# Kernel tuning notes

Hardware: AMD Instinct MI355X
Metric: run time of the kernel (lower is better)

The kernel has to match this reference:

```python
import jax, jax.numpy as jnp
import numpy as np

B, S, IN_DIM = 8, 2048, 8
EMB, HEADS, NCLS = 512, 8, 3
HDIM = EMB // HEADS
HALF = EMB // 2


def setup_inputs() -> dict:
    key = jax.random.key(0)
    ks = jax.random.split(key, 16)
    g = lambda k, shp, fan_in: jax.random.normal(k, shp, jnp.float32) / np.sqrt(fan_in)
    return {
        "features": jax.random.normal(ks[0], (B, S, IN_DIM), jnp.float32),
        "timestamps": jax.random.uniform(ks[1], (B, S, 1), jnp.float32),
        # FeatureEmbedding
        "Wf": g(ks[2], (IN_DIM, EMB), IN_DIM), "bf": jnp.zeros((EMB,), jnp.float32),
        # Time2Vec
        "Wl": g(ks[3], (1, HALF), 1), "bl": jnp.zeros((HALF,), jnp.float32),
        "Wp": g(ks[4], (1, HALF), 1), "bp": jnp.zeros((HALF,), jnp.float32),
        # TimeAwareAttention
        "Wq": g(ks[5], (EMB, EMB), EMB), "bq": jnp.zeros((EMB,), jnp.float32),
        "Wk": g(ks[6], (EMB, EMB), EMB), "bk": jnp.zeros((EMB,), jnp.float32),
        "Wv": g(ks[7], (EMB, EMB), EMB), "bv": jnp.zeros((EMB,), jnp.float32),
        "Wo": g(ks[8], (EMB, EMB), EMB), "bo": jnp.zeros((EMB,), jnp.float32),
        "time_decay": jnp.ones((1,), jnp.float32),
        # Classifier MLP (dropout is identity in eval)
        "W1": g(ks[9], (EMB, EMB // 2), EMB), "b1": jnp.zeros((EMB // 2,), jnp.float32),
        "W2": g(ks[10], (EMB // 2, NCLS), EMB // 2), "b2": jnp.zeros((NCLS,), jnp.float32),
    }


def reference(features, timestamps, Wf, bf, Wl, bl, Wp, bp,
              Wq, bq, Wk, bk, Wv, bv, Wo, bo, time_decay, W1, b1, W2, b2):
    # embeddings: feature linear + Time2Vec(linear || sin(linear))
    feat_emb = features @ Wf + bf                              # [B,S,E]
    time_emb = jnp.concatenate(
        [timestamps @ Wl + bl, jnp.sin(timestamps @ Wp + bp)], axis=-1)
    x = feat_emb + time_emb                                    # [B,S,E]

    # pairwise time-decay weights: exp(-decay * |t_i - t_j|)  [B,S,S]
    t = timestamps[..., 0]
    decay = jnp.exp(-time_decay[0] * jnp.abs(t[:, :, None] - t[:, None, :]))

    def split_heads(y):  # [B,S,E] -> [B,H,S,D]
        return y.reshape(B, S, HEADS, HDIM).transpose(0, 2, 1, 3)

    q = split_heads(x @ Wq + bq)
    k = split_heads(x @ Wk + bk)
    v = split_heads(x @ Wv + bv)

    scores = jnp.einsum('bhsd,bhtd->bhst', q, k) / np.sqrt(HDIM).astype(np.float32)
    scores = scores * decay[:, None, :, :]                     # elementwise decay bias
    attn = jax.nn.softmax(scores, axis=-1)
    out = jnp.einsum('bhst,bhtd->bhsd', attn, v)               # [B,H,S,D]
    out = out.transpose(0, 2, 1, 3).reshape(B, S, EMB)
    out = out @ Wo + bo

    h = out[:, -1, :]                                          # last token
    h = jax.nn.relu(h @ W1 + b1)
    logits = h @ W2 + b2                                       # [B,NCLS]
    return logits
```

## Files before the change

kernel.cpp:

```cpp
#include <hip/hip_runtime.h>
#include <hip/hip_bf16.h>
#include <math.h>

#define B 8
#define S 2048
#define IN_DIM 8
#define EMB 512
#define HEADS 8
#define HDIM 64
#define HALF 256
#define NCLS 3
#define NCHUNK 32

#define WS_KQ    0
#define WS_COEF1 32768
#define WS_PM    33536
#define WS_PS    66304
#define WS_OH    590592
#define WS_OP    594688

__global__ __launch_bounds__(256) void k_head(
    const float* __restrict__ feat, const float* __restrict__ ts,
    const float* __restrict__ Wf, const float* __restrict__ bf,
    const float* __restrict__ Wl, const float* __restrict__ bl,
    const float* __restrict__ Wp, const float* __restrict__ bp,
    const float* __restrict__ Wq, const float* __restrict__ bq,
    const float* __restrict__ Wk, const float* __restrict__ bk,
    float* __restrict__ ws)
{
    const int h = blockIdx.x;
    const int b = blockIdx.y;
    const int bh = b*HEADS + h;
    const int tid = threadIdx.x;
    __shared__ float xl[EMB];
    __shared__ __align__(16) float qc[HDIM];
    __shared__ float kq[EMB];
    __shared__ float red[4][64];
    __shared__ float red10[4][12];

    {
        const float tl = ts[b*S + (S-1)];
        float fv[IN_DIM];
        #pragma unroll
        for (int i = 0; i < IN_DIM; ++i) fv[i] = feat[(b*S + (S-1))*IN_DIM + i];
        #pragma unroll
        for (int r = 0; r < 2; ++r) {
            const int e = tid + r*256;
            float acc = bf[e];
            #pragma unroll
            for (int i = 0; i < IN_DIM; ++i) acc += fv[i]*Wf[i*EMB + e];
            if (r == 0) acc += tl*Wl[e] + bl[e];
            else        acc += __sinf(tl*Wp[e-HALF] + bp[e-HALF]);
            xl[e] = acc;
        }
    }
    __syncthreads();
    {
        const int eo = tid & 63, jq = tid >> 6;
        float acc = (jq == 0) ? bq[h*HDIM + eo] : 0.f;
        #pragma unroll 8
        for (int j = jq*128; j < jq*128 + 128; ++j)
            acc += xl[j]*Wq[j*EMB + h*HDIM + eo];
        red[jq][eo] = acc;
    }
    __syncthreads();
    if (tid < HDIM) qc[tid] = red[0][tid]+red[1][tid]+red[2][tid]+red[3][tid];
    __syncthreads();
    {
        #pragma unroll
        for (int r = 0; r < 2; ++r) {
            const int j = tid + r*256;
            const float4* wr = (const float4*)(Wk + j*EMB + h*HDIM);
            const float4* qv = (const float4*)qc;
            float acc = 0.f;
            #pragma unroll
            for (int k = 0; k < 16; ++k) {
                const float4 w = wr[k], q4 = qv[k];
                acc += w.x*q4.x + w.y*q4.y + w.z*q4.z + w.w*q4.w;
            }
            kq[j] = acc;
            if (j >= HALF) ws[WS_KQ + bh*EMB + j] = acc;
        }
    }
    __syncthreads();
    {
        float a[IN_DIM] = {0.f,0.f,0.f,0.f,0.f,0.f,0.f,0.f};
        float c0 = 0.f, c1 = 0.f;
        #pragma unroll
        for (int r = 0; r < 2; ++r) {
            const int e = tid + r*256;
            const float kv = kq[e];
            #pragma unroll
            for (int i = 0; i < IN_DIM; ++i) a[i] += Wf[i*EMB + e]*kv;
            c0 += bf[e]*kv;
            if (r == 0) { c0 += bl[e]*kv; c1 += Wl[e]*kv; }
        }
        if (tid < HDIM) c0 += qc[tid]*bk[h*HDIM + tid];
        #pragma unroll
        for (int off = 32; off >= 1; off >>= 1) {
            #pragma unroll
            for (int i = 0; i < IN_DIM; ++i) a[i] += __shfl_xor(a[i], off, 64);
            c0 += __shfl_xor(c0, off, 64);
            c1 += __shfl_xor(c1, off, 64);
        }
        const int wid = tid >> 6, lane = tid & 63;
        if (lane == 0) {
            #pragma unroll
            for (int i = 0; i < IN_DIM; ++i) red10[wid][i] = a[i];
            red10[wid][8] = c0; red10[wid][9] = c1;
        }
        __syncthreads();
        if (tid < 10)
            ws[WS_COEF1 + bh*12 + tid] =
                red10[0][tid]+red10[1][tid]+red10[2][tid]+red10[3][tid];
    }
}

__global__ __launch_bounds__(256) void k_part(
    const float* __restrict__ feat, const float* __restrict__ ts,
    const float* __restrict__ Wp, const float* __restrict__ bp,
    const float* __restrict__ tdp, float* __restrict__ ws)
{
    const int c = blockIdx.x;
    const int b = blockIdx.y;
    const int tid = threadIdx.x;
    const int t0 = c*64;

    __shared__ float sin_l[256*65];
    __shared__ __align__(16) float kqh[HEADS][256];
    __shared__ __align__(16) float w_l[64*8];
    __shared__ float tv_l[64];
    __shared__ float f_l[64*9];
    __shared__ float cf[96];

    if (tid < 64) tv_l[tid] = ts[b*S + t0 + tid];
    for (int idx = tid; idx < 64*IN_DIM; idx += 256) {
        const int tt = idx >> 3, i = idx & 7;
        f_l[tt*9 + i] = feat[(b*S + t0 + tt)*IN_DIM + i];
    }
    for (int idx = tid; idx < HEADS*256; idx += 256)
        ((float*)kqh)[idx] = ws[WS_KQ + (b*HEADS + (idx >> 8))*EMB + HALF + (idx & 255)];
    if (tid < 96) cf[tid] = ws[WS_COEF1 + b*96 + tid];
    const float tl = ts[b*S + (S-1)];
    const float td = tdp[0];
    __syncthreads();

    {
        const float wj = Wp[tid], bj = bp[tid];
        float* srow = sin_l + tid*65;
        #pragma unroll 4
        for (int tt = 0; tt < 64; ++tt)
            srow[tt] = __sinf(tv_l[tt]*wj + bj);
    }
    __syncthreads();

    const int t = tid & 63, h0 = tid >> 6;
    const float tv = tv_l[t];
    float fv[IN_DIM];
    #pragma unroll
    for (int i = 0; i < IN_DIM; ++i) fv[i] = f_l[t*9 + i];
    const float dec = __expf(-td*fabsf(tl - tv));
    float sc[2];
    {
        float acc0 = 0.f, acc1 = 0.f;
        const float4* kq0 = (const float4*)&kqh[h0][0];
        const float4* kq1 = (const float4*)&kqh[h0+4][0];
        #pragma unroll 4
        for (int j4 = 0; j4 < 64; ++j4) {
            const float s0 = sin_l[(j4*4+0)*65 + t];
            const float s1 = sin_l[(j4*4+1)*65 + t];
            const float s2 = sin_l[(j4*4+2)*65 + t];
            const float s3 = sin_l[(j4*4+3)*65 + t];
            const float4 ka = kq0[j4], kb = kq1[j4];
            acc0 += s0*ka.x + s1*ka.y + s2*ka.z + s3*ka.w;
            acc1 += s0*kb.x + s1*kb.y + s2*kb.z + s3*kb.w;
        }
        #pragma unroll
        for (int p = 0; p < 2; ++p) {
            const int h = h0 + p*4;
            float base = cf[h*12+8] + tv*cf[h*12+9];
            #pragma unroll
            for (int i = 0; i < IN_DIM; ++i) base += fv[i]*cf[h*12+i];
            sc[p] = (base + ((p == 0) ? acc0 : acc1))*0.125f*dec;
        }
    }
    #pragma unroll
    for (int p = 0; p < 2; ++p) {
        const int h = h0 + p*4;
        float m = sc[p];
        #pragma unroll
        for (int off = 32; off >= 1; off >>= 1) m = fmaxf(m, __shfl_xor(m, off, 64));
        const float w = __expf(sc[p] - m);
        float Z = w, ta = w*tv;
        float fa[IN_DIM];
        #pragma unroll
        for (int i = 0; i < IN_DIM; ++i) fa[i] = w*fv[i];
        #pragma unroll
        for (int off = 32; off >= 1; off >>= 1) {
            Z  += __shfl_xor(Z,  off, 64);
            ta += __shfl_xor(ta, off, 64);
            #pragma unroll
            for (int i = 0; i < IN_DIM; ++i) fa[i] += __shfl_xor(fa[i], off, 64);
        }
        w_l[t*8 + h] = w;
        if (t == 0) {
            float* pm = ws + WS_PM + ((b*NCHUNK + c)*HEADS + h)*16;
            pm[0] = m; pm[1] = Z; pm[2] = ta;
            #pragma unroll
            for (int i = 0; i < IN_DIM; ++i) pm[3+i] = fa[i];
        }
    }
    __syncthreads();
    {
        const int j = tid;
        float accS[HEADS] = {0.f,0.f,0.f,0.f,0.f,0.f,0.f,0.f};
        const float4* wv4 = (const float4*)w_l;
        const float* scol = sin_l + j*65;
        #pragma unroll 4
        for (int tt = 0; tt < 64; ++tt) {
            const float sv = scol[tt];
            const float4 wa = wv4[tt*2], wb = wv4[tt*2+1];
            accS[0] += wa.x*sv; accS[1] += wa.y*sv; accS[2] += wa.z*sv; accS[3] += wa.w*sv;
            accS[4] += wb.x*sv; accS[5] += wb.y*sv; accS[6] += wb.z*sv; accS[7] += wb.w*sv;
        }
        const int base = WS_PS + ((b*NCHUNK + c)*HEADS)*256 + j;
        #pragma unroll
        for (int h = 0; h < HEADS; ++h) ws[base + h*256] = accS[h];
    }
}

__global__ __launch_bounds__(256) void k_ohc(
    const float* __restrict__ Wf, const float* __restrict__ bf,
    const float* __restrict__ Wl, const float* __restrict__ bl,
    const float* __restrict__ Wv, const float* __restrict__ bv,
    const float* __restrict__ ws_, float* __restrict__ ws)
{
    const int h = blockIdx.x;
    const int b = blockIdx.y;
    const int tid = threadIdx.x;
    __shared__ float pm[NCHUNK][12];
    __shared__ float al[NCHUNK];
    __shared__ float cf[10];
    __shared__ float wx[EMB];
    __shared__ float red[4][64];

    for (int idx = tid; idx < NCHUNK*12; idx += 256) {
        const int c = idx / 12, k = idx % 12;
        pm[c][k] = (k < 11) ? ws_[WS_PM + ((b*NCHUNK + c)*HEADS + h)*16 + k] : 0.f;
    }
    __syncthreads();
    float m = pm[0][0];
    #pragma unroll 8
    for (int c = 1; c < NCHUNK; ++c) m = fmaxf(m, pm[c][0]);
    if (tid < NCHUNK) al[tid] = __expf(pm[tid][0] - m);
    __syncthreads();
    float Z = 0.f;
    #pragma unroll 8
    for (int c = 0; c < NCHUNK; ++c) Z += al[c]*pm[c][1];
    const float inv = 1.f/Z;
    if (tid < 9) {
        const int k = (tid == 8) ? 2 : 3 + tid;
        float acc = 0.f;
        #pragma unroll 8
        for (int c = 0; c < NCHUNK; ++c) acc += al[c]*pm[c][k];
        cf[(tid == 8) ? 8 : tid] = acc*inv;
    }
    __syncthreads();
    {
        const int j = tid;
        float acc = 0.f;
        #pragma unroll 8
        for (int c = 0; c < NCHUNK; ++c)
            acc += al[c]*ws_[WS_PS + ((b*NCHUNK + c)*HEADS + h)*256 + j];
        float vh = bf[HALF + j] + acc*inv;
        float vl = bf[j] + cf[8]*Wl[j] + bl[j];
        #pragma unroll
        for (int i = 0; i < IN_DIM; ++i) {
            vh += cf[i]*Wf[i*EMB + HALF + j];
            vl += cf[i]*Wf[i*EMB + j];
        }
        wx[j] = vl;
        wx[HALF + j] = vh;
    }
    __syncthreads();
    {
        const int eo = tid & 63, jq = tid >> 6;
        const int e = h*HDIM + eo;
        float acc = 0.f;
        #pragma unroll 8
        for (int j = jq*128; j < jq*128 + 128; ++j)
            acc += wx[j]*Wv[j*EMB + e];
        red[jq][eo] = acc;
    }
    __syncthreads();
    if (tid < 64)
        ws[WS_OH + b*EMB + h*HDIM + tid] =
            red[0][tid]+red[1][tid]+red[2][tid]+red[3][tid] + bv[h*HDIM + tid];
}

__global__ __launch_bounds__(256) void k_gemv512(
    const float* __restrict__ W, const float* __restrict__ bias,
    float* __restrict__ ws, int in_off, int out_off)
{
    const int ec = blockIdx.x;
    const int b  = blockIdx.y;
    const int tid = threadIdx.x;
    __shared__ float xv[EMB];
    __shared__ float red[4][64];
    xv[tid]       = ws[in_off + b*EMB + tid];
    xv[tid + 256] = ws[in_off + b*EMB + tid + 256];
    __syncthreads();
    {
        const int eo = tid & 63, jq = tid >> 6;
        const int e = ec*64 + eo;
        float acc = 0.f;
        #pragma unroll 8
        for (int j = jq*128; j < jq*128 + 128; ++j)
            acc += xv[j]*W[j*EMB + e];
        red[jq][eo] = acc;
    }
    __syncthreads();
    if (tid < 64)
        ws[out_off + b*EMB + ec*64 + tid] =
            red[0][tid]+red[1][tid]+red[2][tid]+red[3][tid] + bias[ec*64 + tid];
}

__global__ __launch_bounds__(1024) void k_tail(
    const float* __restrict__ W1, const float* __restrict__ b1,
    const float* __restrict__ W2, const float* __restrict__ b2,
    const float* __restrict__ ws, float* __restrict__ out)
{
    const int b = blockIdx.x;
    const int tid = threadIdx.x;
    __shared__ float xv[EMB];
    __shared__ float red[4][HALF];
    __shared__ float red3[4][3];

    if (tid < EMB) xv[tid] = ws[WS_OP + b*EMB + tid];
    __syncthreads();
    {
        const int mm = tid & 255, jq = tid >> 8;
        float acc = 0.f;
        #pragma unroll 8
        for (int j = jq*128; j < jq*128 + 128; ++j)
            acc += xv[j]*W1[j*HALF + mm];
        red[jq][mm] = acc;
    }
    __syncthreads();
    if (tid < HALF) {
        const float hv = fmaxf(red[0][tid]+red[1][tid]+red[2][tid]+red[3][tid] + b1[tid], 0.f);
        float p0 = hv*W2[tid*NCLS + 0];
        float p1 = hv*W2[tid*NCLS + 1];
        float p2 = hv*W2[tid*NCLS + 2];
        #pragma unroll
        for (int off = 32; off >= 1; off >>= 1) {
            p0 += __shfl_xor(p0, off, 64);
            p1 += __shfl_xor(p1, off, 64);
            p2 += __shfl_xor(p2, off, 64);
        }
        const int wid = tid >> 6;
        if ((tid & 63) == 0) { red3[wid][0] = p0; red3[wid][1] = p1; red3[wid][2] = p2; }
    }
    __syncthreads();
    if (tid < NCLS)
        out[b*NCLS + tid] = red3[0][tid]+red3[1][tid]+red3[2][tid]+red3[3][tid] + b2[tid];
}

extern "C" void kernel_launch(void* const* d_in, const int* in_sizes, int n_in,
                              void* d_out, int out_size, void* d_ws, size_t ws_size,
                              hipStream_t stream)
{
    const float* feat = (const float*)d_in[0];
    const float* ts   = (const float*)d_in[1];
    const float* Wf = (const float*)d_in[2];
    const float* bf = (const float*)d_in[3];
    const float* Wl = (const float*)d_in[4];
    const float* bl = (const float*)d_in[5];
    const float* Wp = (const float*)d_in[6];
    const float* bp = (const float*)d_in[7];
    const float* Wq = (const float*)d_in[8];
    const float* bq = (const float*)d_in[9];
    const float* Wk = (const float*)d_in[10];
    const float* bk = (const float*)d_in[11];
    const float* Wv = (const float*)d_in[12];
    const float* bv = (const float*)d_in[13];
    const float* Wo = (const float*)d_in[14];
    const float* bo = (const float*)d_in[15];
    const float* td = (const float*)d_in[16];
    const float* W1 = (const float*)d_in[17];
    const float* b1 = (const float*)d_in[18];
    const float* W2 = (const float*)d_in[19];
    const float* b2 = (const float*)d_in[20];
    float* ws = (float*)d_ws;
    float* out = (float*)d_out;

    hipLaunchKernelGGL(k_head,    dim3(HEADS, B), dim3(256),  0, stream,
                       feat, ts, Wf, bf, Wl, bl, Wp, bp, Wq, bq, Wk, bk, ws);
    hipLaunchKernelGGL(k_part,    dim3(NCHUNK, B),dim3(256),  0, stream,
                       feat, ts, Wp, bp, td, ws);
    hipLaunchKernelGGL(k_ohc,     dim3(HEADS, B), dim3(256),  0, stream,
                       Wf, bf, Wl, bl, Wv, bv, ws, ws);
    hipLaunchKernelGGL(k_gemv512, dim3(8, B),     dim3(256),  0, stream,
                       Wo, bo, ws, WS_OH, WS_OP);
    hipLaunchKernelGGL(k_tail,    dim3(B),        dim3(1024), 0, stream,
                       W1, b1, W2, b2, ws, out);
}
```

Measured before the change: 47.37 us.

## Fuse chunk combine, V/O projections and classifier into one per-batch kernel

Merges the three final kernels (chunk-softmax combine plus V projection, output projection GEMV, MLP tail) into a single 1024-thread kernel with one block per batch. Intermediate vectors stay in shared memory instead of going through global workspace, and two kernel launches are removed. In exchange, the grid shrinks from 64 blocks to 8, so each block streams the full Wv and Wo matrices itself with far less parallelism.

```diff
diff --git a/kernel.cpp b/kernel.cpp
--- a/kernel.cpp
+++ b/kernel.cpp
@@ -16,8 +16,6 @@
 #define WS_COEF1 32768
 #define WS_PM    33536
 #define WS_PS    66304
-#define WS_OH    590592
-#define WS_OP    594688
 
 __global__ __launch_bounds__(256) void k_head(
     const float* __restrict__ feat, const float* __restrict__ ts,
@@ -229,126 +227,115 @@
     }
 }
 
-__global__ __launch_bounds__(256) void k_ohc(
+__global__ __launch_bounds__(1024) void k_cde(
     const float* __restrict__ Wf, const float* __restrict__ bf,
     const float* __restrict__ Wl, const float* __restrict__ bl,
     const float* __restrict__ Wv, const float* __restrict__ bv,
-    const float* __restrict__ ws_, float* __restrict__ ws)
-{
-    const int h = blockIdx.x;
-    const int b = blockIdx.y;
-    const int tid = threadIdx.x;
-    __shared__ float pm[NCHUNK][12];
-    __shared__ float al[NCHUNK];
-    __shared__ float cf[10];
-    __shared__ float wx[EMB];
-    __shared__ float red[4][64];
-
-    for (int idx = tid; idx < NCHUNK*12; idx += 256) {
-        const int c = idx / 12, k = idx % 12;
-        pm[c][k] = (k < 11) ? ws_[WS_PM + ((b*NCHUNK + c)*HEADS + h)*16 + k] : 0.f;
-    }
-    __syncthreads();
-    float m = pm[0][0];
-    #pragma unroll 8
-    for (int c = 1; c < NCHUNK; ++c) m = fmaxf(m, pm[c][0]);
-    if (tid < NCHUNK) al[tid] = __expf(pm[tid][0] - m);
-    __syncthreads();
-    float Z = 0.f;
-    #pragma unroll 8
-    for (int c = 0; c < NCHUNK; ++c) Z += al[c]*pm[c][1];
-    const float inv = 1.f/Z;
-    if (tid < 9) {
-        const int k = (tid == 8) ? 2 : 3 + tid;
-        float acc = 0.f;
-        #pragma unroll 8
-        for (int c = 0; c < NCHUNK; ++c) acc += al[c]*pm[c][k];
-        cf[(tid == 8) ? 8 : tid] = acc*inv;
-    }
-    __syncthreads();
-    {
-        const int j = tid;
-        float acc = 0.f;
-        #pragma unroll 8
-        for (int c = 0; c < NCHUNK; ++c)
-            acc += al[c]*ws_[WS_PS + ((b*NCHUNK + c)*HEADS + h)*256 + j];
-        float vh = bf[HALF + j] + acc*inv;
-        float vl = bf[j] + cf[8]*Wl[j] + bl[j];
-        #pragma unroll
-        for (int i = 0; i < IN_DIM; ++i) {
-            vh += cf[i]*Wf[i*EMB + HALF + j];
-            vl += cf[i]*Wf[i*EMB + j];
-        }
-        wx[j] = vl;
-        wx[HALF + j] = vh;
-    }
-    __syncthreads();
-    {
-        const int eo = tid & 63, jq = tid >> 6;
-        const int e = h*HDIM + eo;
-        float acc = 0.f;
-        #pragma unroll 8
-        for (int j = jq*128; j < jq*128 + 128; ++j)
-            acc += wx[j]*Wv[j*EMB + e];
-        red[jq][eo] = acc;
-    }
-    __syncthreads();
-    if (tid < 64)
-        ws[WS_OH + b*EMB + h*HDIM + tid] =
-            red[0][tid]+red[1][tid]+red[2][tid]+red[3][tid] + bv[h*HDIM + tid];
-}
-
-__global__ __launch_bounds__(256) void k_gemv512(
-    const float* __restrict__ W, const float* __restrict__ bias,
-    float* __restrict__ ws, int in_off, int out_off)
-{
-    const int ec = blockIdx.x;
-    const int b  = blockIdx.y;
-    const int tid = threadIdx.x;
-    __shared__ float xv[EMB];
-    __shared__ float red[4][64];
-    xv[tid]       = ws[in_off + b*EMB + tid];
-    xv[tid + 256] = ws[in_off + b*EMB + tid + 256];
-    __syncthreads();
-    {
-        const int eo = tid & 63, jq = tid >> 6;
-        const int e = ec*64 + eo;
-        float acc = 0.f;
-        #pragma unroll 8
-        for (int j = jq*128; j < jq*128 + 128; ++j)
-            acc += xv[j]*W[j*EMB + e];
-        red[jq][eo] = acc;
-    }
-    __syncthreads();
-    if (tid < 64)
-        ws[out_off + b*EMB + ec*64 + tid] =
-            red[0][tid]+red[1][tid]+red[2][tid]+red[3][tid] + bias[ec*64 + tid];
-}
-
-__global__ __launch_bounds__(1024) void k_tail(
+    const float* __restrict__ Wo, const float* __restrict__ bo,
     const float* __restrict__ W1, const float* __restrict__ b1,
     const float* __restrict__ W2, const float* __restrict__ b2,
     const float* __restrict__ ws, float* __restrict__ out)
 {
     const int b = blockIdx.x;
     const int tid = threadIdx.x;
-    __shared__ float xv[EMB];
-    __shared__ float red[4][HALF];
+    const int g  = tid >> 7;
+    const int tg = tid & 127;
+
+    __shared__ float pmL[HEADS][NCHUNK][12];
+    __shared__ float alL[HEADS][NCHUNK];
+    __shared__ float cfL[HEADS][10];
+    __shared__ float wxL[HEADS][EMB];
+    __shared__ float redL[2][EMB];
+    __shared__ float ohL[EMB];
+    __shared__ float opL[EMB];
+    __shared__ float hhL[HALF];
     __shared__ float red3[4][3];
 
-    if (tid < EMB) xv[tid] = ws[WS_OP + b*EMB + tid];
-    __syncthreads();
+    for (int idx = tg; idx < NCHUNK*11; idx += 128) {
+        const int c = idx / 11, k = idx % 11;
+        pmL[g][c][k] = ws[WS_PM + ((b*NCHUNK + c)*HEADS + g)*16 + k];
+    }
+    __syncthreads();
+    float m = pmL[g][0][0];
+    #pragma unroll 8
+    for (int c = 1; c < NCHUNK; ++c) m = fmaxf(m, pmL[g][c][0]);
+    if (tg < NCHUNK) alL[g][tg] = __expf(pmL[g][tg][0] - m);
+    __syncthreads();
+    float Z = 0.f;
+    #pragma unroll 8
+    for (int c = 0; c < NCHUNK; ++c) Z += alL[g][c]*pmL[g][c][1];
+    const float inv = 1.f/Z;
+    if (tg < 9) {
+        const int k = (tg == 8) ? 2 : 3 + tg;
+        float acc = 0.f;
+        #pragma unroll 8
+        for (int c = 0; c < NCHUNK; ++c) acc += alL[g][c]*pmL[g][c][k];
+        cfL[g][(tg == 8) ? 8 : tg] = acc*inv;
+    }
+    __syncthreads();
+    #pragma unroll
+    for (int r = 0; r < 4; ++r) {
+        const int e = tg + r*128;
+        float val = bf[e];
+        #pragma unroll
+        for (int i = 0; i < IN_DIM; ++i) val += cfL[g][i]*Wf[i*EMB + e];
+        if (e < HALF) {
+            val += cfL[g][8]*Wl[e] + bl[e];
+        } else {
+            const int j = e - HALF;
+            float acc = 0.f;
+            #pragma unroll 8
+            for (int c = 0; c < NCHUNK; ++c)
+                acc += alL[g][c]*ws[WS_PS + ((b*NCHUNK + c)*HEADS + g)*256 + j];
+            val += acc*inv;
+        }
+        wxL[g][e] = val;
+    }
+    __syncthreads();
+
+    {
+        const int e = tid & 511, half = tid >> 9;
+        const int h = e >> 6;
+        float acc = 0.f;
+        #pragma unroll 8
+        for (int j = half*256; j < half*256 + 256; ++j)
+            acc += wxL[h][j]*Wv[j*EMB + e];
+        redL[half][e] = acc;
+    }
+    __syncthreads();
+    if (tid < EMB) ohL[tid] = redL[0][tid] + redL[1][tid] + bv[tid];
+    __syncthreads();
+
+    {
+        const int e = tid & 511, half = tid >> 9;
+        float acc = 0.f;
+        #pragma unroll 8
+        for (int j = half*256; j < half*256 + 256; ++j)
+            acc += ohL[j]*Wo[j*EMB + e];
+        redL[half][e] = acc;
+    }
+    __syncthreads();
+    if (tid < EMB) opL[tid] = redL[0][tid] + redL[1][tid] + bo[tid];
+    __syncthreads();
+
     {
         const int mm = tid & 255, jq = tid >> 8;
         float acc = 0.f;
         #pragma unroll 8
         for (int j = jq*128; j < jq*128 + 128; ++j)
-            acc += xv[j]*W1[j*HALF + mm];
-        red[jq][mm] = acc;
+            acc += opL[j]*W1[j*HALF + mm];
+        ((float*)redL)[jq*HALF + mm] = acc;
     }
     __syncthreads();
     if (tid < HALF) {
-        const float hv = fmaxf(red[0][tid]+red[1][tid]+red[2][tid]+red[3][tid] + b1[tid], 0.f);
+        const float* r4 = (const float*)redL;
+        hhL[tid] = fmaxf(r4[tid] + r4[HALF+tid] + r4[2*HALF+tid] + r4[3*HALF+tid]
+                         + b1[tid], 0.f);
+    }
+    __syncthreads();
+
+    if (tid < HALF) {
+        const float hv = hhL[tid];
         float p0 = hv*W2[tid*NCLS + 0];
         float p1 = hv*W2[tid*NCLS + 1];
         float p2 = hv*W2[tid*NCLS + 2];
@@ -394,14 +381,10 @@
     float* ws = (float*)d_ws;
     float* out = (float*)d_out;
 
-    hipLaunchKernelGGL(k_head,    dim3(HEADS, B), dim3(256),  0, stream,
+    hipLaunchKernelGGL(k_head, dim3(HEADS, B), dim3(256),  0, stream,
                        feat, ts, Wf, bf, Wl, bl, Wp, bp, Wq, bq, Wk, bk, ws);
-    hipLaunchKernelGGL(k_part,    dim3(NCHUNK, B),dim3(256),  0, stream,
+    hipLaunchKernelGGL(k_part, dim3(NCHUNK, B),dim3(256),  0, stream,
                        feat, ts, Wp, bp, td, ws);
-    hipLaunchKernelGGL(k_ohc,     dim3(HEADS, B), dim3(256),  0, stream,
-                       Wf, bf, Wl, bl, Wv, bv, ws, ws);
-    hipLaunchKernelGGL(k_gemv512, dim3(8, B),     dim3(256),  0, stream,
-                       Wo, bo, ws, WS_OH, WS_OP);
-    hipLaunchKernelGGL(k_tail,    dim3(B),        dim3(1024), 0, stream,
-                       W1, b1, W2, b2, ws, out);
+    hipLaunchKernelGGL(k_cde,  dim3(B),        dim3(1024), 0, stream,
+                       Wf, bf, Wl, bl, Wv, bv, Wo, bo, W1, b1, W2, b2, ws, out);
 }
```

New measurement: 61.47 us. +29.7%, slower.

## Halve chunk size for more blocks and fuse Wo projection into per-head kernel

Applied to the files above, without the earlier changes.

The partial-softmax kernel now processes 32 timesteps per block across 64 chunks, one head per 32-lane group, doubling the grid and shrinking shared memory for higher occupancy. The per-head kernel now also applies its head's slice of Wo and writes per-head partial outputs, which the tail kernel sums with the bias. This removes the separate GEMV launch. The cost is more partial data to combine and a larger workspace.

```diff
diff --git a/kernel.cpp b/kernel.cpp
--- a/kernel.cpp
+++ b/kernel.cpp
@@ -10,14 +10,14 @@
 #define HDIM 64
 #define HALF 256
 #define NCLS 3
-#define NCHUNK 32
+#define NCHUNK 64
+#define CT 32
 
 #define WS_KQ    0
 #define WS_COEF1 32768
 #define WS_PM    33536
-#define WS_PS    66304
-#define WS_OH    590592
-#define WS_OP    594688
+#define WS_PS    99072
+#define WS_POP   1147648
 
 __global__ __launch_bounds__(256) void k_head(
     const float* __restrict__ feat, const float* __restrict__ ts,
@@ -124,17 +124,17 @@
     const int c = blockIdx.x;
     const int b = blockIdx.y;
     const int tid = threadIdx.x;
-    const int t0 = c*64;
-
-    __shared__ float sin_l[256*65];
+    const int t0 = c*CT;
+
+    __shared__ float sin_l[256*33];
     __shared__ __align__(16) float kqh[HEADS][256];
-    __shared__ __align__(16) float w_l[64*8];
-    __shared__ float tv_l[64];
-    __shared__ float f_l[64*9];
+    __shared__ __align__(16) float w_l[CT*8];
+    __shared__ float tv_l[CT];
+    __shared__ float f_l[CT*9];
     __shared__ float cf[96];
 
-    if (tid < 64) tv_l[tid] = ts[b*S + t0 + tid];
-    for (int idx = tid; idx < 64*IN_DIM; idx += 256) {
+    if (tid < CT) tv_l[tid] = ts[b*S + t0 + tid];
+    for (int idx = tid; idx < CT*IN_DIM; idx += 256) {
         const int tt = idx >> 3, i = idx & 7;
         f_l[tt*9 + i] = feat[(b*S + t0 + tt)*IN_DIM + i];
     }
@@ -147,56 +147,48 @@
 
     {
         const float wj = Wp[tid], bj = bp[tid];
-        float* srow = sin_l + tid*65;
+        float* srow = sin_l + tid*33;
         #pragma unroll 4
-        for (int tt = 0; tt < 64; ++tt)
+        for (int tt = 0; tt < CT; ++tt)
             srow[tt] = __sinf(tv_l[tt]*wj + bj);
     }
     __syncthreads();
 
-    const int t = tid & 63, h0 = tid >> 6;
+    const int t = tid & (CT-1), h = tid >> 5;
     const float tv = tv_l[t];
     float fv[IN_DIM];
     #pragma unroll
     for (int i = 0; i < IN_DIM; ++i) fv[i] = f_l[t*9 + i];
     const float dec = __expf(-td*fabsf(tl - tv));
-    float sc[2];
-    {
-        float acc0 = 0.f, acc1 = 0.f;
-        const float4* kq0 = (const float4*)&kqh[h0][0];
-        const float4* kq1 = (const float4*)&kqh[h0+4][0];
+    float sc;
+    {
+        float acc = 0.f;
+        const float4* kq4 = (const float4*)&kqh[h][0];
         #pragma unroll 4
         for (int j4 = 0; j4 < 64; ++j4) {
-            const float s0 = sin_l[(j4*4+0)*65 + t];
-            const float s1 = sin_l[(j4*4+1)*65 + t];
-            const float s2 = sin_l[(j4*4+2)*65 + t];
-            const float s3 = sin_l[(j4*4+3)*65 + t];
-            const float4 ka = kq0[j4], kb = kq1[j4];
-            acc0 += s0*ka.x + s1*ka.y + s2*ka.z + s3*ka.w;
-            acc1 += s0*kb.x + s1*kb.y + s2*kb.z + s3*kb.w;
-        }
-        #pragma unroll
-        for (int p = 0; p < 2; ++p) {
-            const int h = h0 + p*4;
-            float base = cf[h*12+8] + tv*cf[h*12+9];
-            #pragma unroll
-            for (int i = 0; i < IN_DIM; ++i) base += fv[i]*cf[h*12+i];
-            sc[p] = (base + ((p == 0) ? acc0 : acc1))*0.125f*dec;
-        }
-    }
-    #pragma unroll
-    for (int p = 0; p < 2; ++p) {
-        const int h = h0 + p*4;
-        float m = sc[p];
-        #pragma unroll
-        for (int off = 32; off >= 1; off >>= 1) m = fmaxf(m, __shfl_xor(m, off, 64));
-        const float w = __expf(sc[p] - m);
+            const float s0 = sin_l[(j4*4+0)*33 + t];
+            const float s1 = sin_l[(j4*4+1)*33 + t];
+            const float s2 = sin_l[(j4*4+2)*33 + t];
+            const float s3 = sin_l[(j4*4+3)*33 + t];
+            const float4 ka = kq4[j4];
+            acc += s0*ka.x + s1*ka.y + s2*ka.z + s3*ka.w;
+        }
+        float base = cf[h*12+8] + tv*cf[h*12+9];
+        #pragma unroll
+        for (int i = 0; i < IN_DIM; ++i) base += fv[i]*cf[h*12+i];
+        sc = (base + acc)*0.125f*dec;
+    }
+    {
+        float m = sc;
+        #pragma unroll
+        for (int off = 16; off >= 1; off >>= 1) m = fmaxf(m, __shfl_xor(m, off, 64));
+        const float w = __expf(sc - m);
         float Z = w, ta = w*tv;
         float fa[IN_DIM];
         #pragma unroll
         for (int i = 0; i < IN_DIM; ++i) fa[i] = w*fv[i];
         #pragma unroll
-        for (int off = 32; off >= 1; off >>= 1) {
+        for (int off = 16; off >= 1; off >>= 1) {
             Z  += __shfl_xor(Z,  off, 64);
             ta += __shfl_xor(ta, off, 64);
             #pragma unroll
@@ -215,9 +207,9 @@
         const int j = tid;
         float accS[HEADS] = {0.f,0.f,0.f,0.f,0.f,0.f,0.f,0.f};
         const float4* wv4 = (const float4*)w_l;
-        const float* scol = sin_l + j*65;
+        const float* scol = sin_l + j*33;
         #pragma unroll 4
-        for (int tt = 0; tt < 64; ++tt) {
+        for (int tt = 0; tt < CT; ++tt) {
             const float sv = scol[tt];
             const float4 wa = wv4[tt*2], wb = wv4[tt*2+1];
             accS[0] += wa.x*sv; accS[1] += wa.y*sv; accS[2] += wa.z*sv; accS[3] += wa.w*sv;
@@ -225,45 +217,46 @@
         }
         const int base = WS_PS + ((b*NCHUNK + c)*HEADS)*256 + j;
         #pragma unroll
-        for (int h = 0; h < HEADS; ++h) ws[base + h*256] = accS[h];
-    }
-}
-
-__global__ __launch_bounds__(256) void k_ohc(
+        for (int hh = 0; hh < HEADS; ++hh) ws[base + hh*256] = accS[hh];
+    }
+}
+
+__global__ __launch_bounds__(256) void k_ohw(
     const float* __restrict__ Wf, const float* __restrict__ bf,
     const float* __restrict__ Wl, const float* __restrict__ bl,
     const float* __restrict__ Wv, const float* __restrict__ bv,
-    const float* __restrict__ ws_, float* __restrict__ ws)
+    const float* __restrict__ Wo, float* __restrict__ ws)
 {
     const int h = blockIdx.x;
     const int b = blockIdx.y;
     const int tid = threadIdx.x;
-    __shared__ float pm[NCHUNK][12];
+    __shared__ float pmL[NCHUNK][12];
     __shared__ float al[NCHUNK];
-    __shared__ float cf[10];
+    __shared__ float cfL[10];
     __shared__ float wx[EMB];
     __shared__ float red[4][64];
-
-    for (int idx = tid; idx < NCHUNK*12; idx += 256) {
-        const int c = idx / 12, k = idx % 12;
-        pm[c][k] = (k < 11) ? ws_[WS_PM + ((b*NCHUNK + c)*HEADS + h)*16 + k] : 0.f;
-    }
-    __syncthreads();
-    float m = pm[0][0];
+    __shared__ __align__(16) float oh_c[HDIM];
+
+    for (int idx = tid; idx < NCHUNK*11; idx += 256) {
+        const int c = idx / 11, k = idx % 11;
+        pmL[c][k] = ws[WS_PM + ((b*NCHUNK + c)*HEADS + h)*16 + k];
+    }
+    __syncthreads();
+    float m = pmL[0][0];
     #pragma unroll 8
-    for (int c = 1; c < NCHUNK; ++c) m = fmaxf(m, pm[c][0]);
-    if (tid < NCHUNK) al[tid] = __expf(pm[tid][0] - m);
+    for (int c = 1; c < NCHUNK; ++c) m = fmaxf(m, pmL[c][0]);
+    if (tid < NCHUNK) al[tid] = __expf(pmL[tid][0] - m);
     __syncthreads();
     float Z = 0.f;
     #pragma unroll 8
-    for (int c = 0; c < NCHUNK; ++c) Z += al[c]*pm[c][1];
+    for (int c = 0; c < NCHUNK; ++c) Z += al[c]*pmL[c][1];
     const float inv = 1.f/Z;
     if (tid < 9) {
         const int k = (tid == 8) ? 2 : 3 + tid;
         float acc = 0.f;
         #pragma unroll 8
-        for (int c = 0; c < NCHUNK; ++c) acc += al[c]*pm[c][k];
-        cf[(tid == 8) ? 8 : tid] = acc*inv;
+        for (int c = 0; c < NCHUNK; ++c) acc += al[c]*pmL[c][k];
+        cfL[(tid == 8) ? 8 : tid] = acc*inv;
     }
     __syncthreads();
     {
@@ -271,13 +264,13 @@
         float acc = 0.f;
         #pragma unroll 8
         for (int c = 0; c < NCHUNK; ++c)
-            acc += al[c]*ws_[WS_PS + ((b*NCHUNK + c)*HEADS + h)*256 + j];
+            acc += al[c]*ws[WS_PS + ((b*NCHUNK + c)*HEADS + h)*256 + j];
         float vh = bf[HALF + j] + acc*inv;
-        float vl = bf[j] + cf[8]*Wl[j] + bl[j];
+        float vl = bf[j] + cfL[8]*Wl[j] + bl[j];
         #pragma unroll
         for (int i = 0; i < IN_DIM; ++i) {
-            vh += cf[i]*Wf[i*EMB + HALF + j];
-            vl += cf[i]*Wf[i*EMB + j];
+            vh += cfL[i]*Wf[i*EMB + HALF + j];
+            vl += cfL[i]*Wf[i*EMB + j];
         }
         wx[j] = vl;
         wx[HALF + j] = vh;
@@ -294,61 +287,56 @@
     }
     __syncthreads();
     if (tid < 64)
-        ws[WS_OH + b*EMB + h*HDIM + tid] =
-            red[0][tid]+red[1][tid]+red[2][tid]+red[3][tid] + bv[h*HDIM + tid];
-}
-
-__global__ __launch_bounds__(256) void k_gemv512(
-    const float* __restrict__ W, const float* __restrict__ bias,
-    float* __restrict__ ws, int in_off, int out_off)
-{
-    const int ec = blockIdx.x;
-    const int b  = blockIdx.y;
-    const int tid = threadIdx.x;
-    __shared__ float xv[EMB];
-    __shared__ float red[4][64];
-    xv[tid]       = ws[in_off + b*EMB + tid];
-    xv[tid + 256] = ws[in_off + b*EMB + tid + 256];
-    __syncthreads();
-    {
-        const int eo = tid & 63, jq = tid >> 6;
-        const int e = ec*64 + eo;
-        float acc = 0.f;
-        #pragma unroll 8
-        for (int j = jq*128; j < jq*128 + 128; ++j)
-            acc += xv[j]*W[j*EMB + e];
-        red[jq][eo] = acc;
-    }
-    __syncthreads();
-    if (tid < 64)
-        ws[out_off + b*EMB + ec*64 + tid] =
-            red[0][tid]+red[1][tid]+red[2][tid]+red[3][tid] + bias[ec*64 + tid];
-}
-
-__global__ __launch_bounds__(1024) void k_tail(
+        oh_c[tid] = red[0][tid]+red[1][tid]+red[2][tid]+red[3][tid] + bv[h*HDIM + tid];
+    __syncthreads();
+    {
+        #pragma unroll
+        for (int r = 0; r < 2; ++r) {
+            const int e = tid + r*256;
+            float acc = 0.f;
+            #pragma unroll 8
+            for (int d = 0; d < HDIM; ++d)
+                acc += oh_c[d]*Wo[(h*HDIM + d)*EMB + e];
+            ws[WS_POP + (b*HEADS + h)*EMB + e] = acc;
+        }
+    }
+}
+
+__global__ __launch_bounds__(1024) void k_tail2(
+    const float* __restrict__ bo,
     const float* __restrict__ W1, const float* __restrict__ b1,
     const float* __restrict__ W2, const float* __restrict__ b2,
     const float* __restrict__ ws, float* __restrict__ out)
 {
     const int b = blockIdx.x;
     const int tid = threadIdx.x;
-    __shared__ float xv[EMB];
+    __shared__ float opL[EMB];
     __shared__ float red[4][HALF];
+    __shared__ float hhL[HALF];
     __shared__ float red3[4][3];
 
-    if (tid < EMB) xv[tid] = ws[WS_OP + b*EMB + tid];
+    if (tid < EMB) {
+        float acc = bo[tid];
+        #pragma unroll
+        for (int h = 0; h < HEADS; ++h)
+            acc += ws[WS_POP + (b*HEADS + h)*EMB + tid];
+        opL[tid] = acc;
+    }
     __syncthreads();
     {
         const int mm = tid & 255, jq = tid >> 8;
         float acc = 0.f;
         #pragma unroll 8
         for (int j = jq*128; j < jq*128 + 128; ++j)
-            acc += xv[j]*W1[j*HALF + mm];
+            acc += opL[j]*W1[j*HALF + mm];
         red[jq][mm] = acc;
     }
     __syncthreads();
+    if (tid < HALF)
+        hhL[tid] = fmaxf(red[0][tid]+red[1][tid]+red[2][tid]+red[3][tid] + b1[tid], 0.f);
+    __syncthreads();
     if (tid < HALF) {
-        const float hv = fmaxf(red[0][tid]+red[1][tid]+red[2][tid]+red[3][tid] + b1[tid], 0.f);
+        const float hv = hhL[tid];
         float p0 = hv*W2[tid*NCLS + 0];
         float p1 = hv*W2[tid*NCLS + 1];
         float p2 = hv*W2[tid*NCLS + 2];
@@ -394,14 +382,12 @@
     float* ws = (float*)d_ws;
     float* out = (float*)d_out;
 
-    hipLaunchKernelGGL(k_head,    dim3(HEADS, B), dim3(256),  0, stream,
+    hipLaunchKernelGGL(k_head,  dim3(HEADS, B),  dim3(256),  0, stream,
                        feat, ts, Wf, bf, Wl, bl, Wp, bp, Wq, bq, Wk, bk, ws);
-    hipLaunchKernelGGL(k_part,    dim3(NCHUNK, B),dim3(256),  0, stream,
+    hipLaunchKernelGGL(k_part,  dim3(NCHUNK, B), dim3(256),  0, stream,
                        feat, ts, Wp, bp, td, ws);
-    hipLaunchKernelGGL(k_ohc,     dim3(HEADS, B), dim3(256),  0, stream,
-                       Wf, bf, Wl, bl, Wv, bv, ws, ws);
-    hipLaunchKernelGGL(k_gemv512, dim3(8, B),     dim3(256),  0, stream,
-                       Wo, bo, ws, WS_OH, WS_OP);
-    hipLaunchKernelGGL(k_tail,    dim3(B),        dim3(1024), 0, stream,
-                       W1, b1, W2, b2, ws, out);
-}
+    hipLaunchKernelGGL(k_ohw,   dim3(HEADS, B),  dim3(256),  0, stream,
+                       Wf, bf, Wl, bl, Wv, bv, Wo, ws);
+    hipLaunchKernelGGL(k_tail2, dim3(B),         dim3(1024), 0, stream,
+                       bo, W1, b1, W2, b2, ws, out);
+}
```

Measured after the change: 48.59 us. +2.6%, slower.
